# Kernel optimization log

Measured on AMD Instinct MI355X. Metric: run time of the kernel, lower is better.

## Reference

```python
import jax, jax.numpy as jnp
import numpy as np

INPUT_DIM = 1024
OUTPUT_DIM = 1024
SPLINE_POINTS = 4

def setup_inputs() -> dict:
    key = jax.random.key(0)
    k1, k2 = jax.random.split(key)
    x = jax.random.normal(k1, (4096, INPUT_DIM), dtype=jnp.float32)
    spline_coeffs = jax.random.normal(k2, (OUTPUT_DIM, INPUT_DIM, SPLINE_POINTS, 4), dtype=jnp.float32)
    return {"x": x, "spline_coeffs": spline_coeffs}

def reference(x, spline_coeffs):
    # Per-feature min-max normalization over the batch dim (as in the torch code,
    # where x[:, j].min()/max() are taken over the batch).
    xmin = jnp.min(x, axis=0, keepdims=True)   # [1, D]
    xmax = jnp.max(x, axis=0, keepdims=True)
    xn = (x - xmin) / (xmax - xmin)            # [B, D]

    # The original sums the cubic polynomial over all spline_points, so the
    # effective coefficients are the sum over the spline_points axis.
    c = jnp.sum(spline_coeffs, axis=2)         # [O, D, 4]

    x2 = xn * xn
    x3 = x2 * xn
    # out[b, o] = sum_d c0*x^3 + c1*x^2 + c2*x + c3
    out = (jnp.einsum('bd,od->bo', x3, c[..., 0])
           + jnp.einsum('bd,od->bo', x2, c[..., 1])
           + jnp.einsum('bd,od->bo', xn, c[..., 2])
           + jnp.sum(c[..., 3], axis=1)[None, :])
    return out
```

## Files before the change

kernel.cpp:

```cpp
#include <hip/hip_runtime.h>
#include <hip/hip_bf16.h>
#include <stdint.h>
#include <stddef.h>

typedef __bf16 bf16;
typedef __attribute__((ext_vector_type(4))) __bf16 bf16x4;
typedef __attribute__((ext_vector_type(8))) __bf16 bf16x8;
typedef __attribute__((ext_vector_type(4))) float f32x4;

#define BATCH 4096
#define DIM 1024
#define ODIM 1024
#define K3 3072

#define WS_CB     0
#define WS_BIAS   6291456
#define WS_PMIN   6295552
#define WS_PMAX   7344128
#define WS_MINV   8392704
#define WS_SCALE  8396800

#define ASYNC16(g, l)                                                          \
  __builtin_amdgcn_global_load_lds(                                            \
      (__attribute__((address_space(1))) void*)(g),                            \
      (__attribute__((address_space(3))) void*)(l), 16, 0, 0)

#define BARRIER()                     \
  do {                                \
    asm volatile("" ::: "memory");    \
    __builtin_amdgcn_s_barrier();     \
    asm volatile("" ::: "memory");    \
  } while (0)
#define WAIT_VM0() __builtin_amdgcn_s_waitcnt(0x0F00 | 0x0070)
#define WAIT_LGKM() __builtin_amdgcn_s_waitcnt(0xC07F)

__global__ void k_stream(const float* __restrict__ x,
                         float* __restrict__ pmin,
                         float* __restrict__ pmax,
                         const float* __restrict__ sp,
                         bf16* __restrict__ CB,
                         float* __restrict__ bias) {
  __shared__ float red[4];
  const int t = threadIdx.x;
  if (blockIdx.x < 256) {
    const int ch = blockIdx.x;
    const float* p = x + (size_t)ch * 16 * DIM + (t << 2);
    f32x4 mn = {1e30f, 1e30f, 1e30f, 1e30f};
    f32x4 mx = {-1e30f, -1e30f, -1e30f, -1e30f};
#pragma unroll
    for (int r = 0; r < 16; ++r) {
      f32x4 v = *(const f32x4*)(p + (size_t)r * DIM);
#pragma unroll
      for (int j = 0; j < 4; ++j) {
        mn[j] = fminf(mn[j], v[j]);
        mx[j] = fmaxf(mx[j], v[j]);
      }
    }
    *(f32x4*)(pmin + ch * DIM + (t << 2)) = mn;
    *(f32x4*)(pmax + ch * DIM + (t << 2)) = mx;
  } else {
    const int o = blockIdx.x - 256;
    const int d = t << 2;
    f32x4 s[4];
#pragma unroll
    for (int dd = 0; dd < 4; ++dd) {
      const float* p = sp + ((size_t)o * DIM + d + dd) * 16;
      f32x4 acc = *(const f32x4*)(p);
      acc += *(const f32x4*)(p + 4);
      acc += *(const f32x4*)(p + 8);
      acc += *(const f32x4*)(p + 12);
      s[dd] = acc;
    }
    size_t cb = (size_t)o * K3 + d;
    bf16x4 c0 = {(bf16)s[0][0], (bf16)s[1][0], (bf16)s[2][0], (bf16)s[3][0]};
    bf16x4 c1 = {(bf16)s[0][1], (bf16)s[1][1], (bf16)s[2][1], (bf16)s[3][1]};
    bf16x4 c2 = {(bf16)s[0][2], (bf16)s[1][2], (bf16)s[2][2], (bf16)s[3][2]};
    *(bf16x4*)(CB + cb) = c0;
    *(bf16x4*)(CB + cb + 1024) = c1;
    *(bf16x4*)(CB + cb + 2048) = c2;
    float v = s[0][3] + s[1][3] + s[2][3] + s[3][3];
#pragma unroll
    for (int off = 32; off > 0; off >>= 1) v += __shfl_down(v, off, 64);
    int lane = t & 63, w = t >> 6;
    if (lane == 0) red[w] = v;
    __syncthreads();
    if (t == 0) bias[o] = red[0] + red[1] + red[2] + red[3];
  }
}

__global__ void k_minmax_final(const float* __restrict__ pmin,
                               const float* __restrict__ pmax,
                               float* __restrict__ minv,
                               float* __restrict__ scale) {
  __shared__ float smn[4][64], smx[4][64];
  const int t = threadIdx.x;
  const int lane = t & 63;
  const int w = t >> 6;
  const int col = blockIdx.x * 64 + lane;
  float mn = 1e30f, mx = -1e30f;
#pragma unroll 8
  for (int ch = w; ch < 256; ch += 4) {
    mn = fminf(mn, pmin[ch * DIM + col]);
    mx = fmaxf(mx, pmax[ch * DIM + col]);
  }
  smn[w][lane] = mn;
  smx[w][lane] = mx;
  __syncthreads();
  if (w == 0) {
    mn = fminf(fminf(smn[0][lane], smn[1][lane]), fminf(smn[2][lane], smn[3][lane]));
    mx = fmaxf(fmaxf(smx[0][lane], smx[1][lane]), fmaxf(smx[2][lane], smx[3][lane]));
    minv[col] = mn;
    scale[col] = 1.0f / (mx - mn);
  }
}

#define MSOFF 98304
#define ABUF(b) ((b) * 24576)
#define BBUF(b) (49152 + (b) * 24576)
__global__ __launch_bounds__(512, 2) void k_gemm(const float* __restrict__ x,
                                                 const float* __restrict__ minv,
                                                 const float* __restrict__ scale,
                                                 const bf16* __restrict__ CBm,
                                                 const float* __restrict__ bias,
                                                 float* __restrict__ out) {
  __shared__ __attribute__((aligned(16))) char smem[106496];

  const int tid = threadIdx.x;
  const int wave = tid >> 6;
  const int lane = tid & 63;

  const int f = blockIdx.x;
  const int chunk = f & 7;
  const int idx = f >> 3;
  const int mt = ((chunk >> 1) << 3) + (idx >> 2);
  const int nt = ((chunk & 1) << 2) + (idx & 3);
  const int bm = mt * 128;
  const int bn = nt * 128;

  const int wr = (wave >> 2) * 64;
  const int wc = (wave & 3) * 32;
  const int mrow = lane & 15;
  const int kq = lane >> 4;

  const int prow = tid >> 2;
  const int u = tid & 3;
  const int aslot = (u ^ ((prow >> 1) & 3)) << 4;
  const float* xg = x + (size_t)(bm + prow) * DIM + u * 8;

  const char* gBp = (const char*)CBm + (size_t)(bn + (tid >> 2)) * 6144 +
                    (size_t)(((tid & 3) ^ ((tid >> 3) & 3)) << 4);

  if (tid < 256) {
    f32x4 m = *(const f32x4*)(minv + tid * 4);
    *(f32x4*)(smem + MSOFF + tid * 16) = m;
  } else {
    f32x4 s = *(const f32x4*)(scale + (tid - 256) * 4);
    *(f32x4*)(smem + MSOFF + 4096 + (tid - 256) * 16) = s;
  }

  f32x4 xa, xb;
#define LOADX(dtv)                                                            \
  do {                                                                        \
    xa = *(const f32x4*)(xg + (dtv) * 32);                                    \
    xb = *(const f32x4*)(xg + (dtv) * 32 + 4);                                \
  } while (0)

#define STAGE_B(buf, dtv)                                                     \
  do {                                                                        \
    const char* gb_ = gBp + (size_t)(dtv) * 64;                               \
    char* lb_ = smem + BBUF(buf) + wave * 1024;                               \
    ASYNC16(gb_, lb_);                                                        \
    ASYNC16(gb_ + 2048, lb_ + 8192);                                          \
    ASYNC16(gb_ + 4096, lb_ + 16384);                                         \
  } while (0)

#define POWERS_WRITE(abuf, dtv)                                               \
  do {                                                                        \
    const char* msp = smem + MSOFF + ((dtv) * 32 + u * 8) * 4;                \
    f32x4 mn0 = *(const f32x4*)(msp);                                         \
    f32x4 mn1 = *(const f32x4*)(msp + 16);                                    \
    f32x4 sc0 = *(const f32x4*)(msp + 4096);                                  \
    f32x4 sc1 = *(const f32x4*)(msp + 4112);                                  \
    f32x4 n0 = (xa - mn0) * sc0, n1 = (xb - mn1) * sc1;                       \
    f32x4 q0 = n0 * n0, q1 = n1 * n1;                                         \
    f32x4 c0v = q0 * n0, c1v = q1 * n1;                                       \
    bf16x8 w1, w2, w3;                                                        \
    _Pragma("unroll") for (int e = 0; e < 4; ++e) {                           \
      w3[e] = (bf16)c0v[e]; w3[e + 4] = (bf16)c1v[e];                         \
      w2[e] = (bf16)q0[e];  w2[e + 4] = (bf16)q1[e];                          \
      w1[e] = (bf16)n0[e];  w1[e + 4] = (bf16)n1[e];                          \
    }                                                                         \
    char* aw_ = smem + ABUF(abuf) + prow * 64 + aslot;                        \
    *(bf16x8*)(aw_) = w3;                                   \
    *(bf16x8*)(aw_ + 8192) = w2;                            \
    *(bf16x8*)(aw_ + 16384) = w1;                           \
  } while (0)

  f32x4 acc[4][2] = {};

#define COMPUTE(buf)                                                          \
  do {                                                                        \
    const char* ab_ = smem + ABUF(buf);                                       \
    const char* bb_ = smem + BBUF(buf);                                       \
    _Pragma("unroll") for (int p = 0; p < 3; ++p) {                           \
      bf16x8 bg[2];                                                           \
      _Pragma("unroll") for (int j = 0; j < 2; ++j) {                         \
        int rowb = wc + j * 16 + mrow;                                        \
        bg[j] = *(const bf16x8*)(bb_ + p * 8192 + rowb * 64 +                 \
                                 ((kq ^ ((rowb >> 1) & 3)) << 4));            \
      }                                                                       \
      bf16x8 af[4];                                                           \
      _Pragma("unroll") for (int i = 0; i < 4; ++i) {                         \
        int rowa = wr + i * 16 + mrow;                                        \
        af[i] = *(const bf16x8*)(ab_ + p * 8192 + rowa * 64 +                 \
                                 ((kq ^ ((rowa >> 1) & 3)) << 4));            \
      }                                                                       \
      _Pragma("unroll") for (int i = 0; i < 4; ++i)                           \
          _Pragma("unroll") for (int j = 0; j < 2; ++j)                       \
              acc[i][j] = __builtin_amdgcn_mfma_f32_16x16x32_bf16(            \
                  af[i], bg[j], acc[i][j], 0, 0, 0);                          \
    }                                                                         \
  } while (0)

  STAGE_B(0, 0);
  LOADX(0);
  WAIT_VM0();
  WAIT_LGKM();
  BARRIER();
  POWERS_WRITE(0, 0);
  LOADX(1);
  WAIT_LGKM();
  BARRIER();

#pragma unroll 2
  for (int dt = 0; dt < 32; ++dt) {
    if (dt < 31) STAGE_B((dt + 1) & 1, dt + 1);
    COMPUTE(dt & 1);
    if (dt < 31) POWERS_WRITE((dt + 1) & 1, dt + 1);
    WAIT_VM0();
    if (dt < 30) LOADX(dt + 2);
    WAIT_LGKM();
    BARRIER();
  }

  const int ccol = lane & 15;
  const int crow = (lane >> 4) * 4;
#pragma unroll
  for (int j = 0; j < 2; ++j) {
    const int col = bn + wc + j * 16 + ccol;
    const float bv = bias[col];
#pragma unroll
    for (int i = 0; i < 4; ++i) {
      const int row0 = bm + wr + i * 16 + crow;
#pragma unroll
      for (int r = 0; r < 4; ++r)
        out[(size_t)(row0 + r) * ODIM + col] = acc[i][j][r] + bv;
    }
  }
#undef LOADX
#undef STAGE_B
#undef POWERS_WRITE
#undef COMPUTE
}

extern "C" void kernel_launch(void* const* d_in, const int* in_sizes, int n_in,
                              void* d_out, int out_size, void* d_ws, size_t ws_size,
                              hipStream_t stream) {
  (void)in_sizes; (void)n_in; (void)out_size; (void)ws_size;
  const float* x = (const float*)d_in[0];
  const float* sp = (const float*)d_in[1];
  float* out = (float*)d_out;
  char* ws = (char*)d_ws;

  bf16* CBm = (bf16*)(ws + WS_CB);
  float* bias = (float*)(ws + WS_BIAS);
  float* pmin = (float*)(ws + WS_PMIN);
  float* pmax = (float*)(ws + WS_PMAX);
  float* minv = (float*)(ws + WS_MINV);
  float* scale = (float*)(ws + WS_SCALE);

  k_stream<<<1280, 256, 0, stream>>>(x, pmin, pmax, sp, CBm, bias);
  k_minmax_final<<<16, 256, 0, stream>>>(pmin, pmax, minv, scale);
  k_gemm<<<256, 512, 0, stream>>>(x, minv, scale, CBm, bias, out);
}
```

Before: 151.1 us.

## Shrink GEMM tile to 128x64 with 256-thread blocks and 512 workgroups

The GEMM kernel moves from 128x128 tiles with 512 threads to 128x64 tiles with 256 threads, doubling the grid to 512 blocks and cutting LDS use. Each thread now normalizes and packs 16 x elements instead of 8. The last-iteration barrier is also skipped. The goal is better CU occupancy and balance across 256 CUs, at the cost of recomputing the A-side powers twice as often, once per N tile.

Result: slower. 159.2 us (+5.4%).

```diff
diff --git a/kernel.cpp b/kernel.cpp
--- a/kernel.cpp
+++ b/kernel.cpp
@@ -114,16 +114,16 @@
   }
 }
 
-#define MSOFF 98304
 #define ABUF(b) ((b) * 24576)
-#define BBUF(b) (49152 + (b) * 24576)
-__global__ __launch_bounds__(512, 2) void k_gemm(const float* __restrict__ x,
+#define BBUF(b) (49152 + (b) * 12288)
+#define MSOFF   73728
+__global__ __launch_bounds__(256, 2) void k_gemm(const float* __restrict__ x,
                                                  const float* __restrict__ minv,
                                                  const float* __restrict__ scale,
                                                  const bf16* __restrict__ CBm,
                                                  const float* __restrict__ bias,
                                                  float* __restrict__ out) {
-  __shared__ __attribute__((aligned(16))) char smem[106496];
+  __shared__ __attribute__((aligned(16))) char smem[81920];
 
   const int tid = threadIdx.x;
   const int wave = tid >> 6;
@@ -132,68 +132,72 @@
   const int f = blockIdx.x;
   const int chunk = f & 7;
   const int idx = f >> 3;
-  const int mt = ((chunk >> 1) << 3) + (idx >> 2);
-  const int nt = ((chunk & 1) << 2) + (idx & 3);
+  const int mt = ((chunk >> 1) << 3) + (idx >> 3);
+  const int nt = ((chunk & 1) << 3) + (idx & 7);
   const int bm = mt * 128;
-  const int bn = nt * 128;
-
-  const int wr = (wave >> 2) * 64;
-  const int wc = (wave & 3) * 32;
+  const int bn = nt * 64;
+
+  const int wr = (wave >> 1) * 64;
+  const int wc = (wave & 1) * 32;
   const int mrow = lane & 15;
   const int kq = lane >> 4;
 
-  const int prow = tid >> 2;
-  const int u = tid & 3;
-  const int aslot = (u ^ ((prow >> 1) & 3)) << 4;
-  const float* xg = x + (size_t)(bm + prow) * DIM + u * 8;
-
-  const char* gBp = (const char*)CBm + (size_t)(bn + (tid >> 2)) * 6144 +
-                    (size_t)(((tid & 3) ^ ((tid >> 3) & 3)) << 4);
-
-  if (tid < 256) {
-    f32x4 m = *(const f32x4*)(minv + tid * 4);
-    *(f32x4*)(smem + MSOFF + tid * 16) = m;
-  } else {
-    f32x4 s = *(const f32x4*)(scale + (tid - 256) * 4);
-    *(f32x4*)(smem + MSOFF + 4096 + (tid - 256) * 16) = s;
-  }
-
-  f32x4 xa, xb;
+  const int pr = tid >> 1;
+  const int h = tid & 1;
+  const int sA0 = ((h * 2 + 0) ^ ((pr >> 1) & 3)) << 4;
+  const int sA1 = ((h * 2 + 1) ^ ((pr >> 1) & 3)) << 4;
+  const float* xg = x + (size_t)(bm + pr) * DIM + h * 16;
+
+  const int brow = tid >> 2;
+  const int bus = (tid & 3) ^ ((tid >> 3) & 3);
+  const char* gB = (const char*)CBm + (size_t)(bn + brow) * 6144 + bus * 16;
+  const int ldsB = wave * 1024;
+
+  f32x4 xv0, xv1, xv2, xv3;
 #define LOADX(dtv)                                                            \
   do {                                                                        \
-    xa = *(const f32x4*)(xg + (dtv) * 32);                                    \
-    xb = *(const f32x4*)(xg + (dtv) * 32 + 4);                                \
+    const float* xp_ = xg + (dtv) * 32;                                       \
+    xv0 = *(const f32x4*)(xp_);                                               \
+    xv1 = *(const f32x4*)(xp_ + 4);                                           \
+    xv2 = *(const f32x4*)(xp_ + 8);                                           \
+    xv3 = *(const f32x4*)(xp_ + 12);                                          \
   } while (0)
 
 #define STAGE_B(buf, dtv)                                                     \
   do {                                                                        \
-    const char* gb_ = gBp + (size_t)(dtv) * 64;                               \
-    char* lb_ = smem + BBUF(buf) + wave * 1024;                               \
+    const char* gb_ = gB + (size_t)(dtv) * 64;                                \
+    char* lb_ = smem + BBUF(buf) + ldsB;                                      \
     ASYNC16(gb_, lb_);                                                        \
-    ASYNC16(gb_ + 2048, lb_ + 8192);                                          \
-    ASYNC16(gb_ + 4096, lb_ + 16384);                                         \
-  } while (0)
-
-#define POWERS_WRITE(abuf, dtv)                                               \
-  do {                                                                        \
-    const char* msp = smem + MSOFF + ((dtv) * 32 + u * 8) * 4;                \
-    f32x4 mn0 = *(const f32x4*)(msp);                                         \
-    f32x4 mn1 = *(const f32x4*)(msp + 16);                                    \
-    f32x4 sc0 = *(const f32x4*)(msp + 4096);                                  \
-    f32x4 sc1 = *(const f32x4*)(msp + 4112);                                  \
-    f32x4 n0 = (xa - mn0) * sc0, n1 = (xb - mn1) * sc1;                       \
-    f32x4 q0 = n0 * n0, q1 = n1 * n1;                                         \
-    f32x4 c0v = q0 * n0, c1v = q1 * n1;                                       \
-    bf16x8 w1, w2, w3;                                                        \
-    _Pragma("unroll") for (int e = 0; e < 4; ++e) {                           \
-      w3[e] = (bf16)c0v[e]; w3[e + 4] = (bf16)c1v[e];                         \
-      w2[e] = (bf16)q0[e];  w2[e + 4] = (bf16)q1[e];                          \
-      w1[e] = (bf16)n0[e];  w1[e + 4] = (bf16)n1[e];                          \
-    }                                                                         \
-    char* aw_ = smem + ABUF(abuf) + prow * 64 + aslot;                        \
-    *(bf16x8*)(aw_) = w3;                                   \
-    *(bf16x8*)(aw_ + 8192) = w2;                            \
-    *(bf16x8*)(aw_ + 16384) = w1;                           \
+    ASYNC16(gb_ + 2048, lb_ + 4096);                                          \
+    ASYNC16(gb_ + 4096, lb_ + 8192);                                          \
+  } while (0)
+
+#define PK8(lo, hi, dst)                                                      \
+  _Pragma("unroll") for (int e_ = 0; e_ < 4; ++e_) {                          \
+    dst[e_] = (bf16)lo[e_];                                                   \
+    dst[e_ + 4] = (bf16)hi[e_];                                               \
+  }
+
+#define POWERS(buf, dtv)                                                      \
+  do {                                                                        \
+    const char* msp = smem + MSOFF + ((dtv) * 32 + h * 16) * 4;               \
+    f32x4 n0 = (xv0 - *(const f32x4*)(msp)) * *(const f32x4*)(msp + 4096);    \
+    f32x4 n1 = (xv1 - *(const f32x4*)(msp + 16)) * *(const f32x4*)(msp + 4112); \
+    f32x4 n2 = (xv2 - *(const f32x4*)(msp + 32)) * *(const f32x4*)(msp + 4128); \
+    f32x4 n3 = (xv3 - *(const f32x4*)(msp + 48)) * *(const f32x4*)(msp + 4144); \
+    f32x4 q0 = n0 * n0, q1 = n1 * n1, q2 = n2 * n2, q3 = n3 * n3;             \
+    f32x4 c0 = q0 * n0, c1 = q1 * n1, c2 = q2 * n2, c3 = q3 * n3;             \
+    bf16x8 w3a, w3b, w2a, w2b, w1a, w1b;                                      \
+    PK8(c0, c1, w3a) PK8(c2, c3, w3b)                                         \
+    PK8(q0, q1, w2a) PK8(q2, q3, w2b)                                         \
+    PK8(n0, n1, w1a) PK8(n2, n3, w1b)                                         \
+    char* aw_ = smem + ABUF(buf) + pr * 64;                                   \
+    *(bf16x8*)(aw_ + sA0) = w3a;                                              \
+    *(bf16x8*)(aw_ + sA1) = w3b;                                              \
+    *(bf16x8*)(aw_ + 8192 + sA0) = w2a;                                       \
+    *(bf16x8*)(aw_ + 8192 + sA1) = w2b;                                       \
+    *(bf16x8*)(aw_ + 16384 + sA0) = w1a;                                      \
+    *(bf16x8*)(aw_ + 16384 + sA1) = w1b;                                      \
   } while (0)
 
   f32x4 acc[4][2] = {};
@@ -203,13 +207,12 @@
     const char* ab_ = smem + ABUF(buf);                                       \
     const char* bb_ = smem + BBUF(buf);                                       \
     _Pragma("unroll") for (int p = 0; p < 3; ++p) {                           \
-      bf16x8 bg[2];                                                           \
+      bf16x8 af[4], bg[2];                                                    \
       _Pragma("unroll") for (int j = 0; j < 2; ++j) {                         \
         int rowb = wc + j * 16 + mrow;                                        \
-        bg[j] = *(const bf16x8*)(bb_ + p * 8192 + rowb * 64 +                 \
+        bg[j] = *(const bf16x8*)(bb_ + p * 4096 + rowb * 64 +                 \
                                  ((kq ^ ((rowb >> 1) & 3)) << 4));            \
       }                                                                       \
-      bf16x8 af[4];                                                           \
       _Pragma("unroll") for (int i = 0; i < 4; ++i) {                         \
         int rowa = wr + i * 16 + mrow;                                        \
         af[i] = *(const bf16x8*)(ab_ + p * 8192 + rowa * 64 +                 \
@@ -222,25 +225,34 @@
     }                                                                         \
   } while (0)
 
+  {
+    f32x4 m = *(const f32x4*)(minv + tid * 4);
+    f32x4 s = *(const f32x4*)(scale + tid * 4);
+    *(f32x4*)(smem + MSOFF + tid * 16) = m;
+    *(f32x4*)(smem + MSOFF + 4096 + tid * 16) = s;
+  }
   STAGE_B(0, 0);
   LOADX(0);
   WAIT_VM0();
   WAIT_LGKM();
   BARRIER();
-  POWERS_WRITE(0, 0);
+  POWERS(0, 0);
   LOADX(1);
   WAIT_LGKM();
   BARRIER();
 
 #pragma unroll 2
   for (int dt = 0; dt < 32; ++dt) {
-    if (dt < 31) STAGE_B((dt + 1) & 1, dt + 1);
-    COMPUTE(dt & 1);
-    if (dt < 31) POWERS_WRITE((dt + 1) & 1, dt + 1);
-    WAIT_VM0();
-    if (dt < 30) LOADX(dt + 2);
-    WAIT_LGKM();
-    BARRIER();
+    const int cur = dt & 1;
+    if (dt < 31) STAGE_B(cur ^ 1, dt + 1);
+    COMPUTE(cur);
+    if (dt < 31) {
+      POWERS(cur ^ 1, dt + 1);
+      WAIT_VM0();
+      if (dt < 30) LOADX(dt + 2);
+      WAIT_LGKM();
+      BARRIER();
+    }
   }
 
   const int ccol = lane & 15;
@@ -259,7 +271,8 @@
   }
 #undef LOADX
 #undef STAGE_B
-#undef POWERS_WRITE
+#undef PK8
+#undef POWERS
 #undef COMPUTE
 }
 
@@ -281,5 +294,5 @@
 
   k_stream<<<1280, 256, 0, stream>>>(x, pmin, pmax, sp, CBm, bias);
   k_minmax_final<<<16, 256, 0, stream>>>(pmin, pmax, minv, scale);
-  k_gemm<<<256, 512, 0, stream>>>(x, minv, scale, CBm, bias, out);
-}
+  k_gemm<<<512, 256, 0, stream>>>(x, minv, scale, CBm, bias, out);
+}
```
